# Performance work log

Measured on AMD Instinct MI355X. Metric: run time of the kernel, lower is better.

## Reference

```python
import jax, jax.numpy as jnp
import numpy as np

N, E, G = 50000, 640000, 512
F_NODE, F_EDGE, HID, H, L = 8, 3, 128, 4, 4
C = HID // H


def setup_inputs() -> dict:
    key = jax.random.key(0)
    ks = jax.random.split(key, 24)
    p = lambda k, s: jax.random.normal(k, s, jnp.float32) * 0.1
    return {
        "x": jax.random.normal(ks[0], (N, F_NODE), jnp.float32),
        "edge_attr": jax.random.normal(ks[1], (E, F_EDGE), jnp.float32),
        "edge_index": jax.random.randint(ks[2], (2, E), 0, N, dtype=jnp.int32),
        "batch": jnp.sort(jax.random.randint(ks[3], (N,), 0, G, dtype=jnp.int32)),
        "enc_node_w": p(ks[4], (F_NODE, HID)), "enc_node_b": p(ks[5], (HID,)),
        "enc_edge_w": p(ks[6], (F_EDGE, HID)), "enc_edge_b": p(ks[7], (HID,)),
        "gat_lin_w": p(ks[8], (L, HID, HID)),
        "gat_att_src": p(ks[9], (L, H, C)),
        "gat_att_dst": p(ks[10], (L, H, C)),
        "gat_lin_edge_w": p(ks[11], (L, HID, HID)),
        "gat_att_edge": p(ks[12], (L, H, C)),
        "gat_bias": p(ks[13], (L, HID)),
        "bn_gamma": jnp.ones((L, HID), jnp.float32),
        "bn_beta": jnp.zeros((L, HID), jnp.float32),
        "fc1_w": p(ks[14], (HID, HID)), "fc1_b": p(ks[15], (HID,)),
        "fc2_w": p(ks[16], (HID, HID // 2)), "fc2_b": p(ks[17], (HID // 2,)),
        "fc3_w": p(ks[18], (HID // 2, 1)), "fc3_b": p(ks[19], (1,)),
    }


def _gat(x, src, dst, ea, lin_w, a_src, a_dst, lin_e_w, a_edge, bias):
    # PyG GATConv (concat=True, negative_slope=0.2, edge_dim=HID)
    xp = (x @ lin_w).reshape(N, H, C)                      # [N,H,C]
    s = jnp.einsum('nhc,hc->nh', xp, a_src)                # alpha_src per node
    d = jnp.einsum('nhc,hc->nh', xp, a_dst)                # alpha_dst per node
    ep = (ea @ lin_e_w).reshape(-1, H, C)                  # [Et,H,C]
    e = jnp.einsum('ehc,hc->eh', ep, a_edge)               # alpha_edge per edge
    alpha = jax.nn.leaky_relu(s[src] + d[dst] + e, 0.2)    # [Et,H]
    # segment softmax over incoming edges of each target node
    m = jax.ops.segment_max(alpha, dst, num_segments=N)
    w = jnp.exp(alpha - m[dst])
    z = jax.ops.segment_sum(w, dst, num_segments=N)
    w = w / (z[dst] + 1e-16)
    msg = xp[src] * w[:, :, None]                          # [Et,H,C]
    out = jax.ops.segment_sum(msg, dst, num_segments=N)
    return out.reshape(N, HID) + bias


def reference(x, edge_attr, edge_index, batch,
              enc_node_w, enc_node_b, enc_edge_w, enc_edge_b,
              gat_lin_w, gat_att_src, gat_att_dst, gat_lin_edge_w, gat_att_edge, gat_bias,
              bn_gamma, bn_beta, fc1_w, fc1_b, fc2_w, fc2_b, fc3_w, fc3_b):
    src, dst = edge_index[0], edge_index[1]
    h = x @ enc_node_w + enc_node_b
    ea = edge_attr @ enc_edge_w + enc_edge_b
    # add_self_loops with fill_value='mean': self-loop attr = mean of incoming edge attrs
    deg = jax.ops.segment_sum(jnp.ones((E,), h.dtype), dst, num_segments=N)
    loop_ea = jax.ops.segment_sum(ea, dst, num_segments=N) / jnp.maximum(deg, 1.0)[:, None]
    loop = jnp.arange(N, dtype=src.dtype)
    src_f = jnp.concatenate([src, loop])
    dst_f = jnp.concatenate([dst, loop])
    ea_f = jnp.concatenate([ea, loop_ea], axis=0)
    for i in range(L):
        hn = _gat(h, src_f, dst_f, ea_f, gat_lin_w[i], gat_att_src[i], gat_att_dst[i],
                  gat_lin_edge_w[i], gat_att_edge[i], gat_bias[i])
        mu = hn.mean(0)
        var = ((hn - mu) ** 2).mean(0)                     # BatchNorm1d training-mode stats
        hn = (hn - mu) / jnp.sqrt(var + 1e-5) * bn_gamma[i] + bn_beta[i]
        hn = jax.nn.relu(hn)
        h = h + hn if i > 0 else hn
    # global mean pool over graphs
    cnt = jax.ops.segment_sum(jnp.ones((N,), h.dtype), batch, num_segments=G)
    g = jax.ops.segment_sum(h, batch, num_segments=G) / jnp.maximum(cnt, 1.0)[:, None]
    g = jax.nn.relu(g @ fc1_w + fc1_b)
    g = jax.nn.relu(g @ fc2_w + fc2_b)
    return g @ fc3_w + fc3_b
```

## Files before the change

kernel.cpp:

```cpp
#include <hip/hip_runtime.h>
#include <hip/hip_bf16.h>

#define NN 50000
#define EE 640000
#define ET (EE + NN)
#define GG 512
#define NPB 16
#define NLB 3125
#define CPX 391
#define ECAP 768
#define WSTR (ECAP + 4)

typedef unsigned int uint;
typedef __attribute__((ext_vector_type(8))) short short8;
typedef __attribute__((ext_vector_type(4))) float floatx4;

__device__ inline float2 bf2f(uint u) {
    return make_float2(__uint_as_float(u << 16), __uint_as_float(u & 0xffff0000u));
}
__device__ inline uint packbf(float a, float b) {
    __hip_bfloat162 t;
    t.x = __float2bfloat16(a);
    t.y = __float2bfloat16(b);
    return *(uint*)&t;
}

__global__ __launch_bounds__(256) void k_prep(const float* __restrict__ lin_e_w,
                                              const float* __restrict__ att_e,
                                              const float* __restrict__ encW,
                                              const float* __restrict__ encB,
                                              const float* __restrict__ W,
                                              float* __restrict__ Mt, float* __restrict__ bns4,
                                              uint* __restrict__ WbT) {
    int tid = threadIdx.x;
    if (blockIdx.x == 0) {
        __shared__ float we[128 * 16];
        for (int idx = tid; idx < 2048; idx += 256) {
            int k = idx >> 4, lh = idx & 15, l = lh >> 2, h = lh & 3;
            const float* wrow = lin_e_w + l * 16384 + k * 128 + h * 32;
            const float* arow = att_e + l * 128 + h * 32;
            float acc = 0.f;
#pragma unroll
            for (int c = 0; c < 32; c++) acc += wrow[c] * arow[c];
            we[k * 16 + lh] = acc;
        }
        for (int i = tid; i < 4 * 8 * 256; i += 256) bns4[i] = 0.f;
        __syncthreads();
        if (tid < 64) {
            int lh = tid >> 2, r = tid & 3;
            float acc = 0.f;
            for (int k = 0; k < 128; k++) {
                float a = (r < 3) ? encW[r * 128 + k] : encB[k];
                acc += a * we[k * 16 + lh];
            }
            Mt[lh * 4 + r] = acc;
        }
    } else {
        int idx = (blockIdx.x - 1) * 256 + tid;
        if (idx >= 4 * 128 * 64) return;
        int l = idx >> 13, rem = idx & 8191, n = rem >> 6, u = rem & 63;
        const float* Wl = W + l * 16384;
        WbT[idx] = packbf(Wl[(2 * u) * 128 + n], Wl[(2 * u + 1) * 128 + n]);
    }
}

__global__ __launch_bounds__(256) void k_enc(const float* __restrict__ x,
                                             const float* __restrict__ W,
                                             const float* __restrict__ b,
                                             uint* __restrict__ hb) {
    int idx = blockIdx.x * 256 + threadIdx.x;
    if (idx >= NN * 64) return;
    int n = idx >> 6, c0 = (idx & 63) * 2;
    float a0 = b[c0], a1 = b[c0 + 1];
    const float* xr = x + n * 8;
#pragma unroll
    for (int f = 0; f < 8; f++) {
        a0 += xr[f] * W[f * 128 + c0];
        a1 += xr[f] * W[f * 128 + c0 + 1];
    }
    hb[idx] = packbf(a0, a1);
}

__global__ __launch_bounds__(256) void k_deg(const int* __restrict__ dst, int* __restrict__ deg) {
    int e0 = (blockIdx.x * 256 + threadIdx.x) * 4;
    if (e0 >= EE) return;
    int4 d4 = *(const int4*)(dst + e0);
    atomicAdd(&deg[d4.x], 1);
    atomicAdd(&deg[d4.y], 1);
    atomicAdd(&deg[d4.z], 1);
    atomicAdd(&deg[d4.w], 1);
}

__global__ __launch_bounds__(1024) void k_scan(const int* __restrict__ deg, int* __restrict__ rp,
                                               int* __restrict__ fill) {
    __shared__ int wsum[16];
    __shared__ int carry_sh;
    int tid = threadIdx.x, lane = tid & 63, wid = tid >> 6;
    if (tid == 0) { carry_sh = 0; rp[0] = 0; }
    __syncthreads();
    for (int base = 0; base < NN; base += 8192) {
        int i0 = base + tid * 8;
        int v[8], p[8];
        if (i0 < NN) {
            int4 a = *(const int4*)(deg + i0);
            int4 bq = *(const int4*)(deg + i0 + 4);
            v[0] = a.x + 1; v[1] = a.y + 1; v[2] = a.z + 1; v[3] = a.w + 1;
            v[4] = bq.x + 1; v[5] = bq.y + 1; v[6] = bq.z + 1; v[7] = bq.w + 1;
        } else {
#pragma unroll
            for (int u = 0; u < 8; u++) v[u] = 0;
        }
        int run = 0;
#pragma unroll
        for (int u = 0; u < 8; u++) { run += v[u]; p[u] = run; }
        int xv = run;
        for (int off = 1; off < 64; off <<= 1) {
            int s = __shfl_up(xv, off);
            if (lane >= off) xv += s;
        }
        if (lane == 63) wsum[wid] = xv;
        __syncthreads();
        if (wid == 0 && lane < 16) {
            int s = wsum[lane];
            for (int off = 1; off < 16; off <<= 1) {
                int u = __shfl_up(s, off);
                if (lane >= off) s += u;
            }
            wsum[lane] = s;
        }
        __syncthreads();
        int excl = carry_sh + (wid > 0 ? wsum[wid - 1] : 0) + xv - run;
        if (i0 < NN) {
#pragma unroll
            for (int u = 0; u < 8; u++) {
                rp[i0 + u + 1] = excl + p[u];
                fill[i0 + u] = excl + (u ? p[u - 1] : 0);
            }
        }
        __syncthreads();
        if (tid == 0) carry_sh += wsum[15];
        __syncthreads();
    }
}

__global__ __launch_bounds__(256) void k_fill(const int* __restrict__ src, const int* __restrict__ dst,
                                              const float* __restrict__ edge_attr,
                                              int* __restrict__ fill, int* __restrict__ ed) {
    int e0 = (blockIdx.x * 256 + threadIdx.x) * 4;
    if (e0 >= EE) return;
    int4 d4 = *(const int4*)(dst + e0);
    int4 s4 = *(const int4*)(src + e0);
    const float* ar = edge_attr + (size_t)e0 * 3;
    float4 f0 = *(const float4*)(ar + 0);
    float4 f1 = *(const float4*)(ar + 4);
    float4 f2 = *(const float4*)(ar + 8);
    int p0 = atomicAdd(&fill[d4.x], 1);
    int p1 = atomicAdd(&fill[d4.y], 1);
    int p2 = atomicAdd(&fill[d4.z], 1);
    int p3 = atomicAdd(&fill[d4.w], 1);
    *(int4*)(ed + (size_t)p0 * 4) = make_int4(s4.x, __float_as_int(f0.x), __float_as_int(f0.y), __float_as_int(f0.z));
    *(int4*)(ed + (size_t)p1 * 4) = make_int4(s4.y, __float_as_int(f0.w), __float_as_int(f1.x), __float_as_int(f1.y));
    *(int4*)(ed + (size_t)p2 * 4) = make_int4(s4.z, __float_as_int(f1.z), __float_as_int(f1.w), __float_as_int(f2.x));
    *(int4*)(ed + (size_t)p3 * 4) = make_int4(s4.w, __float_as_int(f2.y), __float_as_int(f2.z), __float_as_int(f2.w));
}

__global__ __launch_bounds__(256) void k_selfloop(const int* __restrict__ rp, int* __restrict__ ed) {
    int t = blockIdx.x * 256 + threadIdx.x;
    int n = t >> 4, sub = t & 15;
    if (n >= NN) return;
    int b = rp[n], en = rp[n + 1];
    int d = en - b - 1;
    float s0 = 0.f, s1 = 0.f, s2 = 0.f;
    for (int j = sub; j < d; j += 16) {
        int4 r = *(const int4*)(ed + (size_t)(b + j) * 4);
        s0 += __int_as_float(r.y); s1 += __int_as_float(r.z); s2 += __int_as_float(r.w);
    }
#pragma unroll
    for (int off = 8; off; off >>= 1) {
        s0 += __shfl_xor(s0, off, 16);
        s1 += __shfl_xor(s1, off, 16);
        s2 += __shfl_xor(s2, off, 16);
    }
    if (sub == 0) {
        float inv = 1.f / fmaxf((float)d, 1.f);
        *(int4*)(ed + (size_t)(en - 1) * 4) =
            make_int4(n, __float_as_int(s0 * inv), __float_as_int(s1 * inv), __float_as_int(s2 * inv));
    }
}

__global__ __launch_bounds__(256) void k_gemm(const uint* __restrict__ hb, const uint* __restrict__ WbT,
                                              const float* __restrict__ a_src, const float* __restrict__ a_dst,
                                              uint* __restrict__ xpb, float* __restrict__ s_arr,
                                              float* __restrict__ d_arr) {
    __shared__ __align__(16) uint Bl[128 * 68];
    int tid = threadIdx.x;
    for (int idx = tid; idx < 2048; idx += 256) {
        int n = idx >> 4, u4 = idx & 15;
        uint4 v = *(const uint4*)(WbT + n * 64 + u4 * 4);
        *(uint4*)(&Bl[n * 68 + u4 * 4]) = v;
    }
    int lane = tid & 63, wv = tid >> 6;
    int ln15 = lane & 15, quad = lane >> 4;
    int rowBase = blockIdx.x * 64 + wv * 16;
    int rowA = rowBase + ln15;
    int rowAc = rowA < NN ? rowA : 0;
    __syncthreads();
    short8 af[4];
#pragma unroll
    for (int c = 0; c < 4; c++)
        af[c] = *(const short8*)((const short*)hb + (size_t)rowAc * 128 + c * 32 + quad * 8);
    floatx4 acc[8];
#pragma unroll
    for (int t = 0; t < 8; t++) acc[t] = (floatx4){0.f, 0.f, 0.f, 0.f};
#pragma unroll
    for (int c = 0; c < 4; c++) {
#pragma unroll
        for (int t = 0; t < 8; t++) {
            short8 bf = *(const short8*)((const short*)&Bl[(16 * t + ln15) * 68] + c * 32 + quad * 8);
            acc[t] = __builtin_amdgcn_mfma_f32_16x16x32_bf16(af[c], bf, acc[t], 0, 0, 0);
        }
    }
#pragma unroll
    for (int t = 0; t < 8; t++) {
#pragma unroll
        for (int r = 0; r < 4; r++) {
            float v = acc[t][r];
            float vhi = __shfl_xor(v, 1);
            int grow = rowBase + quad * 4 + r;
            if (!(ln15 & 1) && grow < NN)
                xpb[(size_t)grow * 64 + 8 * t + (ln15 >> 1)] = packbf(v, vhi);
        }
    }
    float asl[4], ash[4], adl[4], adh[4];
#pragma unroll
    for (int hh = 0; hh < 4; hh++) {
        asl[hh] = a_src[hh * 32 + ln15]; ash[hh] = a_src[hh * 32 + 16 + ln15];
        adl[hh] = a_dst[hh * 32 + ln15]; adh[hh] = a_dst[hh * 32 + 16 + ln15];
    }
#pragma unroll
    for (int r = 0; r < 4; r++) {
        float s0 = acc[0][r] * asl[0] + acc[1][r] * ash[0];
        float s1 = acc[2][r] * asl[1] + acc[3][r] * ash[1];
        float s2 = acc[4][r] * asl[2] + acc[5][r] * ash[2];
        float s3 = acc[6][r] * asl[3] + acc[7][r] * ash[3];
        float d0 = acc[0][r] * adl[0] + acc[1][r] * adh[0];
        float d1 = acc[2][r] * adl[1] + acc[3][r] * adh[1];
        float d2 = acc[4][r] * adl[2] + acc[5][r] * adh[2];
        float d3 = acc[6][r] * adl[3] + acc[7][r] * adh[3];
#pragma unroll
        for (int off = 1; off < 16; off <<= 1) {
            s0 += __shfl_xor(s0, off); s1 += __shfl_xor(s1, off);
            s2 += __shfl_xor(s2, off); s3 += __shfl_xor(s3, off);
            d0 += __shfl_xor(d0, off); d1 += __shfl_xor(d1, off);
            d2 += __shfl_xor(d2, off); d3 += __shfl_xor(d3, off);
        }
        int grow = rowBase + quad * 4 + r;
        if (ln15 == 0 && grow < NN) {
            *(float4*)(s_arr + grow * 4) = make_float4(s0, s1, s2, s3);
            *(float4*)(d_arr + grow * 4) = make_float4(d0, d1, d2, d3);
        }
    }
}

__global__ __launch_bounds__(256) void k_edge(const int* __restrict__ rp, const int* __restrict__ ed,
                                              const float* __restrict__ Mt,
                                              const float* __restrict__ s_arr, const float* __restrict__ d_arr,
                                              const uint* __restrict__ xpb, uint* __restrict__ outb,
                                              float* __restrict__ bns, int layer) {
    __shared__ int rps[NPB + 1];
    __shared__ float d4c[NPB][4];
    __shared__ __align__(16) float shw[4][WSTR];
    __shared__ int shs[ECAP];
    int tid = threadIdx.x;
    int lb = (blockIdx.x & 7) * CPX + (blockIdx.x >> 3);
    if (lb >= NLB) return;
    int nb0 = lb * NPB;
    if (tid <= NPB) rps[tid] = rp[nb0 + tid];
    if (tid < NPB * 4)
        d4c[tid >> 2][tid & 3] = d_arr[(size_t)(nb0 + (tid >> 2)) * 4 + (tid & 3)];
    float4 mt0 = *(const float4*)(Mt + (layer * 4 + 0) * 4);
    float4 mt1 = *(const float4*)(Mt + (layer * 4 + 1) * 4);
    float4 mt2 = *(const float4*)(Mt + (layer * 4 + 2) * 4);
    float4 mt3 = *(const float4*)(Mt + (layer * 4 + 3) * 4);
    __syncthreads();
    int e0 = rps[0], e1 = rps[NPB];
    int e1c = e1 - e0 > ECAP ? e0 + ECAP : e1;
    for (int s = e0 + tid; s < e1c; s += 256) {
        int lo = 0, hi = NPB - 1;
        while (lo < hi) { int mid = (lo + hi) >> 1; if (rps[mid + 1] <= s) lo = mid + 1; else hi = mid; }
        int ni = lo;
        int4 r = *(const int4*)(ed + (size_t)s * 4);
        int sv = r.x;
        float a0 = __int_as_float(r.y), a1 = __int_as_float(r.z), a2 = __int_as_float(r.w);
        int kni = rps[ni + 1] - rps[ni];
        float wf = (s == rps[ni + 1] - 1) ? (kni > 1 ? 1.f : 0.f) : 1.f;
        float4 s4 = *(const float4*)(s_arr + (size_t)sv * 4);
        float e_0 = a0 * mt0.x + a1 * mt0.y + a2 * mt0.z + wf * mt0.w;
        float e_1 = a0 * mt1.x + a1 * mt1.y + a2 * mt1.z + wf * mt1.w;
        float e_2 = a0 * mt2.x + a1 * mt2.y + a2 * mt2.z + wf * mt2.w;
        float e_3 = a0 * mt3.x + a1 * mt3.y + a2 * mt3.z + wf * mt3.w;
        float al0 = s4.x + d4c[ni][0] + e_0; al0 = al0 > 0.f ? al0 : 0.2f * al0;
        float al1 = s4.y + d4c[ni][1] + e_1; al1 = al1 > 0.f ? al1 : 0.2f * al1;
        float al2 = s4.z + d4c[ni][2] + e_2; al2 = al2 > 0.f ? al2 : 0.2f * al2;
        float al3 = s4.w + d4c[ni][3] + e_3; al3 = al3 > 0.f ? al3 : 0.2f * al3;
        int ls = s - e0;
        shs[ls] = sv;
        shw[0][ls] = __expf(al0);
        shw[1][ls] = __expf(al1);
        shw[2][ls] = __expf(al2);
        shw[3][ls] = __expf(al3);
    }
    __syncthreads();
    int wv = tid >> 6, lane = tid & 63, hh = lane >> 4;
    float4 mth = hh == 0 ? mt0 : hh == 1 ? mt1 : hh == 2 ? mt2 : mt3;
    float bs0 = 0.f, bs1 = 0.f, bq0 = 0.f, bq1 = 0.f;
#pragma unroll
    for (int q = 0; q < 4; q++) {
        int ni = wv * 4 + q;
        int startg = rps[ni];
        int start = startg - e0;
        int k = rps[ni + 1] - startg;
        float acc0 = 0.f, acc1 = 0.f, z = 0.f;
        int kc = ECAP - start;
        kc = kc < 0 ? 0 : (kc > k ? k : kc);
        int j = 0;
        for (; j + 4 <= kc; j += 4) {
            int s0 = shs[start + j], s1 = shs[start + j + 1];
            int s2 = shs[start + j + 2], s3 = shs[start + j + 3];
            float w0 = shw[hh][start + j], w1 = shw[hh][start + j + 1];
            float w2 = shw[hh][start + j + 2], w3 = shw[hh][start + j + 3];
            z += w0 + w1 + w2 + w3;
            uint x0 = xpb[(size_t)s0 * 64 + lane];
            uint x1 = xpb[(size_t)s1 * 64 + lane];
            uint x2 = xpb[(size_t)s2 * 64 + lane];
            uint x3 = xpb[(size_t)s3 * 64 + lane];
            float2 f0 = bf2f(x0), f1 = bf2f(x1), f2 = bf2f(x2), f3 = bf2f(x3);
            acc0 += w0 * f0.x + w1 * f1.x + w2 * f2.x + w3 * f3.x;
            acc1 += w0 * f0.y + w1 * f1.y + w2 * f2.y + w3 * f3.y;
        }
        for (; j < kc; j++) {
            float w = shw[hh][start + j];
            int sv = shs[start + j];
            z += w;
            float2 f = bf2f(xpb[(size_t)sv * 64 + lane]);
            acc0 += w * f.x; acc1 += w * f.y;
        }
        for (; j < k; j++) {
            int sg = startg + j;
            int4 r = *(const int4*)(ed + (size_t)sg * 4);
            int sv = r.x;
            float a0 = __int_as_float(r.y), a1 = __int_as_float(r.z), a2 = __int_as_float(r.w);
            float wf = (j < k - 1) ? 1.f : (k > 1 ? 1.f : 0.f);
            float sva = s_arr[(size_t)sv * 4 + hh];
            float ev = a0 * mth.x + a1 * mth.y + a2 * mth.z + wf * mth.w;
            float a = sva + d4c[ni][hh] + ev; a = a > 0.f ? a : 0.2f * a;
            float w = __expf(a);
            z += w;
            float2 f = bf2f(xpb[(size_t)sv * 64 + lane]);
            acc0 += w * f.x; acc1 += w * f.y;
        }
        float zi = 1.f / (z + 1e-16f);
        float o0 = acc0 * zi, o1 = acc1 * zi;
        outb[(size_t)(nb0 + ni) * 64 + lane] = packbf(o0, o1);
        bs0 += o0; bs1 += o1; bq0 += o0 * o0; bq1 += o1 * o1;
    }
    __syncthreads();
    float* scratch = &shw[0][0];
    scratch[wv * 256 + lane * 4 + 0] = bs0;
    scratch[wv * 256 + lane * 4 + 1] = bs1;
    scratch[wv * 256 + lane * 4 + 2] = bq0;
    scratch[wv * 256 + lane * 4 + 3] = bq1;
    __syncthreads();
    float v = scratch[tid] + scratch[256 + tid] + scratch[512 + tid] + scratch[768 + tid];
    int ln = tid >> 2, st = tid & 3;
    int gidx = (st < 2) ? (2 * ln + st) : (128 + 2 * ln + (st - 2));
    atomicAdd(&bns[(blockIdx.x & 7) * 256 + gidx], v);
}

__global__ __launch_bounds__(256) void k_norm(const uint* __restrict__ xb, const float* __restrict__ sums,
                                              const float* __restrict__ gamma, const float* __restrict__ beta,
                                              uint* __restrict__ hb, int first) {
    __shared__ float sc[128], sf[128];
    int tid = threadIdx.x;
    if (tid < 128) {
        float s = 0.f, q = 0.f;
#pragma unroll
        for (int k = 0; k < 8; k++) { s += sums[k * 256 + tid]; q += sums[k * 256 + 128 + tid]; }
        float mu = s * (1.f / NN);
        float var = q * (1.f / NN) - mu * mu;
        float iv = rsqrtf(fmaxf(var, 0.f) + 1e-5f);
        float a = gamma[tid] * iv;
        sc[tid] = a;
        sf[tid] = beta[tid] - mu * a;
    }
    __syncthreads();
    int idx = blockIdx.x * 256 + tid;
    if (idx >= NN * 64) return;
    int c0 = (idx & 63) * 2;
    float2 v2 = bf2f(xb[idx]);
    float r0 = fmaxf(v2.x * sc[c0] + sf[c0], 0.f);
    float r1 = fmaxf(v2.y * sc[c0 + 1] + sf[c0 + 1], 0.f);
    if (!first) {
        float2 hp = bf2f(hb[idx]);
        r0 += hp.x; r1 += hp.y;
    }
    hb[idx] = packbf(r0, r1);
}

__global__ __launch_bounds__(256) void k_pool(const uint* __restrict__ hb, const int* __restrict__ batch,
                                              float* __restrict__ g) {
    int t = threadIdx.x & 63, rh = threadIdx.x >> 6;
    int gi = blockIdx.x;
    int lo = 0, hi = NN;
    while (lo < hi) { int mid = (lo + hi) >> 1; if (batch[mid] < gi) lo = mid + 1; else hi = mid; }
    int start = lo;
    hi = NN;
    while (lo < hi) { int mid = (lo + hi) >> 1; if (batch[mid] < gi + 1) lo = mid + 1; else hi = mid; }
    int end = lo;
    float s0 = 0.f, s1 = 0.f;
    for (int n = start + rh; n < end; n += 4) {
        float2 v = bf2f(hb[(size_t)n * 64 + t]);
        s0 += v.x; s1 += v.y;
    }
    __shared__ float sh[2][256];
    sh[0][threadIdx.x] = s0; sh[1][threadIdx.x] = s1;
    __syncthreads();
    if (rh == 0) {
        float inv = 1.f / fmaxf((float)(end - start), 1.f);
        g[gi * 128 + 2 * t]     = (sh[0][t] + sh[0][64 + t] + sh[0][128 + t] + sh[0][192 + t]) * inv;
        g[gi * 128 + 2 * t + 1] = (sh[1][t] + sh[1][64 + t] + sh[1][128 + t] + sh[1][192 + t]) * inv;
    }
}

__global__ __launch_bounds__(128) void k_fc(const float* __restrict__ g,
                                            const float* __restrict__ w1, const float* __restrict__ b1,
                                            const float* __restrict__ w2, const float* __restrict__ b2,
                                            const float* __restrict__ w3, const float* __restrict__ b3,
                                            float* __restrict__ out) {
    __shared__ float gv[128];
    __shared__ float h1[128];
    __shared__ float h2[64];
    int gi = blockIdx.x, t = threadIdx.x;
    gv[t] = g[gi * 128 + t];
    __syncthreads();
    float acc = b1[t];
    for (int kk = 0; kk < 128; kk++) acc += gv[kk] * w1[kk * 128 + t];
    h1[t] = fmaxf(acc, 0.f);
    __syncthreads();
    if (t < 64) {
        float a2 = b2[t];
        for (int kk = 0; kk < 128; kk++) a2 += h1[kk] * w2[kk * 64 + t];
        h2[t] = fmaxf(a2, 0.f);
    }
    __syncthreads();
    if (t < 64) {
        float p = h2[t] * w3[t];
#pragma unroll
        for (int off = 32; off; off >>= 1) p += __shfl_xor(p, off);
        if (t == 0) out[gi] = p + b3[0];
    }
}

extern "C" void kernel_launch(void* const* d_in, const int* in_sizes, int n_in,
                              void* d_out, int out_size, void* d_ws, size_t ws_size,
                              hipStream_t stream) {
    const float* x            = (const float*)d_in[0];
    const float* edge_attr    = (const float*)d_in[1];
    const int*   edge_index   = (const int*)d_in[2];
    const int*   batch        = (const int*)d_in[3];
    const float* enc_node_w   = (const float*)d_in[4];
    const float* enc_node_b   = (const float*)d_in[5];
    const float* enc_edge_w   = (const float*)d_in[6];
    const float* enc_edge_b   = (const float*)d_in[7];
    const float* gat_lin_w    = (const float*)d_in[8];
    const float* gat_att_src  = (const float*)d_in[9];
    const float* gat_att_dst  = (const float*)d_in[10];
    const float* gat_lin_edge = (const float*)d_in[11];
    const float* gat_att_edge = (const float*)d_in[12];
    const float* bn_gamma     = (const float*)d_in[14];
    const float* bn_beta      = (const float*)d_in[15];
    const float* fc1_w        = (const float*)d_in[16];
    const float* fc1_b        = (const float*)d_in[17];
    const float* fc2_w        = (const float*)d_in[18];
    const float* fc2_b        = (const float*)d_in[19];
    const float* fc3_w        = (const float*)d_in[20];
    const float* fc3_b        = (const float*)d_in[21];
    float* outv = (float*)d_out;

    char* ws = (char*)d_ws;
    size_t off = 0;
    auto alloc = [&](size_t bytes) -> void* {
        void* p = ws + off;
        off = (off + bytes + 255) & ~(size_t)255;
        return p;
    };
    uint*  hbv     = (uint*)alloc((size_t)NN * 64 * 4);
    uint*  goutb   = (uint*)alloc((size_t)NN * 64 * 4);
    uint*  xpb     = (uint*)alloc((size_t)NN * 64 * 4);
    float* s_arr   = (float*)alloc((size_t)NN * 4 * 4);
    float* d_arr   = (float*)alloc((size_t)NN * 4 * 4);
    int*   deg     = (int*)alloc((size_t)NN * 4);
    int*   fill    = (int*)alloc((size_t)NN * 4);
    int*   rp      = (int*)alloc((size_t)(NN + 1) * 4);
    int*   ed      = (int*)alloc((size_t)ET * 4 * 4);
    uint*  WbT     = (uint*)alloc((size_t)4 * 128 * 64 * 4);
    float* Mt      = (float*)alloc(64 * 4);
    float* bns4    = (float*)alloc((size_t)4 * 8 * 256 * 4);
    float* g       = (float*)alloc((size_t)GG * 128 * 4);
    (void)ws_size; (void)in_sizes; (void)n_in; (void)out_size;

    hipMemsetAsync(deg, 0, NN * 4, stream);

    const int* srce = edge_index;
    const int* dste = edge_index + EE;

    k_prep<<<1 + (4 * 128 * 64 + 255) / 256, 256, 0, stream>>>(gat_lin_edge, gat_att_edge,
                                                               enc_edge_w, enc_edge_b, gat_lin_w,
                                                               Mt, bns4, WbT);
    k_enc<<<(NN * 64 + 255) / 256, 256, 0, stream>>>(x, enc_node_w, enc_node_b, hbv);
    k_deg<<<(EE / 4 + 255) / 256, 256, 0, stream>>>(dste, deg);
    k_scan<<<1, 1024, 0, stream>>>(deg, rp, fill);
    k_fill<<<(EE / 4 + 255) / 256, 256, 0, stream>>>(srce, dste, edge_attr, fill, ed);
    k_selfloop<<<(NN * 16 + 255) / 256, 256, 0, stream>>>(rp, ed);

    for (int l = 0; l < 4; l++) {
        k_gemm<<<(NN + 63) / 64, 256, 0, stream>>>(hbv, WbT + l * 8192,
                                                   gat_att_src + l * 128, gat_att_dst + l * 128,
                                                   xpb, s_arr, d_arr);
        k_edge<<<8 * CPX, 256, 0, stream>>>(rp, ed, Mt, s_arr, d_arr, xpb, goutb,
                                            bns4 + l * 2048, l);
        k_norm<<<(NN * 64 + 255) / 256, 256, 0, stream>>>(goutb, bns4 + l * 2048, bn_gamma + l * 128,
                                                          bn_beta + l * 128, hbv, l == 0 ? 1 : 0);
    }

    k_pool<<<GG, 256, 0, stream>>>(hbv, batch, g);
    k_fc<<<GG, 128, 0, stream>>>(g, fc1_w, fc1_b, fc2_w, fc2_b, fc3_w, fc3_b, outv);
}
```

Baseline: 484.6 us.

## Fuse BatchNorm/residual into next GEMM and pooling/FC tail, merge encoder into prep

Removes the per-layer k_norm pass by applying BatchNorm, ReLU and the residual add inside the next layer's GEMM prologue, which also writes the updated hidden state and stages it in shared memory. The last layer's normalisation is fused into a combined pooling+MLP kernel, and the node encoder is folded into the prep kernel. The degree and fill kernels now process 8 edges per thread. Together this cuts kernel launches and one full read/write pass over node features per layer. In exchange the GEMM needs more shared memory and the tail recomputes the normalisation while reading two arrays.

```diff
diff --git a/kernel.cpp b/kernel.cpp
--- a/kernel.cpp
+++ b/kernel.cpp
@@ -30,10 +30,14 @@
                                               const float* __restrict__ encW,
                                               const float* __restrict__ encB,
                                               const float* __restrict__ W,
+                                              const float* __restrict__ x,
+                                              const float* __restrict__ nodeW,
+                                              const float* __restrict__ nodeB,
                                               float* __restrict__ Mt, float* __restrict__ bns4,
-                                              uint* __restrict__ WbT) {
+                                              uint* __restrict__ WbT, uint* __restrict__ hb) {
     int tid = threadIdx.x;
-    if (blockIdx.x == 0) {
+    int blk = blockIdx.x;
+    if (blk == 0) {
         __shared__ float we[128 * 16];
         for (int idx = tid; idx < 2048; idx += 256) {
             int k = idx >> 4, lh = idx & 15, l = lh >> 2, h = lh & 3;
@@ -55,40 +59,34 @@
             }
             Mt[lh * 4 + r] = acc;
         }
-    } else {
-        int idx = (blockIdx.x - 1) * 256 + tid;
-        if (idx >= 4 * 128 * 64) return;
+    } else if (blk <= 128) {
+        int idx = (blk - 1) * 256 + tid;
         int l = idx >> 13, rem = idx & 8191, n = rem >> 6, u = rem & 63;
         const float* Wl = W + l * 16384;
         WbT[idx] = packbf(Wl[(2 * u) * 128 + n], Wl[(2 * u + 1) * 128 + n]);
-    }
-}
-
-__global__ __launch_bounds__(256) void k_enc(const float* __restrict__ x,
-                                             const float* __restrict__ W,
-                                             const float* __restrict__ b,
-                                             uint* __restrict__ hb) {
-    int idx = blockIdx.x * 256 + threadIdx.x;
-    if (idx >= NN * 64) return;
-    int n = idx >> 6, c0 = (idx & 63) * 2;
-    float a0 = b[c0], a1 = b[c0 + 1];
-    const float* xr = x + n * 8;
-#pragma unroll
-    for (int f = 0; f < 8; f++) {
-        a0 += xr[f] * W[f * 128 + c0];
-        a1 += xr[f] * W[f * 128 + c0 + 1];
-    }
-    hb[idx] = packbf(a0, a1);
+    } else {
+        int idx = (blk - 129) * 256 + tid;
+        if (idx >= NN * 64) return;
+        int n = idx >> 6, c0 = (idx & 63) * 2;
+        float a0 = nodeB[c0], a1 = nodeB[c0 + 1];
+        const float* xr = x + n * 8;
+#pragma unroll
+        for (int f = 0; f < 8; f++) {
+            a0 += xr[f] * nodeW[f * 128 + c0];
+            a1 += xr[f] * nodeW[f * 128 + c0 + 1];
+        }
+        hb[idx] = packbf(a0, a1);
+    }
 }
 
 __global__ __launch_bounds__(256) void k_deg(const int* __restrict__ dst, int* __restrict__ deg) {
-    int e0 = (blockIdx.x * 256 + threadIdx.x) * 4;
+    int e0 = (blockIdx.x * 256 + threadIdx.x) * 8;
     if (e0 >= EE) return;
-    int4 d4 = *(const int4*)(dst + e0);
-    atomicAdd(&deg[d4.x], 1);
-    atomicAdd(&deg[d4.y], 1);
-    atomicAdd(&deg[d4.z], 1);
-    atomicAdd(&deg[d4.w], 1);
+    int4 d0 = *(const int4*)(dst + e0), d1 = *(const int4*)(dst + e0 + 4);
+    atomicAdd(&deg[d0.x], 1); atomicAdd(&deg[d0.y], 1);
+    atomicAdd(&deg[d0.z], 1); atomicAdd(&deg[d0.w], 1);
+    atomicAdd(&deg[d1.x], 1); atomicAdd(&deg[d1.y], 1);
+    atomicAdd(&deg[d1.z], 1); atomicAdd(&deg[d1.w], 1);
 }
 
 __global__ __launch_bounds__(1024) void k_scan(const int* __restrict__ deg, int* __restrict__ rp,
@@ -146,22 +144,25 @@
 __global__ __launch_bounds__(256) void k_fill(const int* __restrict__ src, const int* __restrict__ dst,
                                               const float* __restrict__ edge_attr,
                                               int* __restrict__ fill, int* __restrict__ ed) {
-    int e0 = (blockIdx.x * 256 + threadIdx.x) * 4;
+    int e0 = (blockIdx.x * 256 + threadIdx.x) * 8;
     if (e0 >= EE) return;
-    int4 d4 = *(const int4*)(dst + e0);
-    int4 s4 = *(const int4*)(src + e0);
-    const float* ar = edge_attr + (size_t)e0 * 3;
-    float4 f0 = *(const float4*)(ar + 0);
-    float4 f1 = *(const float4*)(ar + 4);
-    float4 f2 = *(const float4*)(ar + 8);
-    int p0 = atomicAdd(&fill[d4.x], 1);
-    int p1 = atomicAdd(&fill[d4.y], 1);
-    int p2 = atomicAdd(&fill[d4.z], 1);
-    int p3 = atomicAdd(&fill[d4.w], 1);
-    *(int4*)(ed + (size_t)p0 * 4) = make_int4(s4.x, __float_as_int(f0.x), __float_as_int(f0.y), __float_as_int(f0.z));
-    *(int4*)(ed + (size_t)p1 * 4) = make_int4(s4.y, __float_as_int(f0.w), __float_as_int(f1.x), __float_as_int(f1.y));
-    *(int4*)(ed + (size_t)p2 * 4) = make_int4(s4.z, __float_as_int(f1.z), __float_as_int(f1.w), __float_as_int(f2.x));
-    *(int4*)(ed + (size_t)p3 * 4) = make_int4(s4.w, __float_as_int(f2.y), __float_as_int(f2.z), __float_as_int(f2.w));
+    int4 d0 = *(const int4*)(dst + e0), d1 = *(const int4*)(dst + e0 + 4);
+    int4 s0 = *(const int4*)(src + e0), s1 = *(const int4*)(src + e0 + 4);
+    const float4* ar4 = (const float4*)(edge_attr + (size_t)e0 * 3);
+    float4 q[6];
+#pragma unroll
+    for (int i = 0; i < 6; i++) q[i] = ar4[i];
+    const float* a = (const float*)q;
+    int dd[8] = {d0.x, d0.y, d0.z, d0.w, d1.x, d1.y, d1.z, d1.w};
+    int ss[8] = {s0.x, s0.y, s0.z, s0.w, s1.x, s1.y, s1.z, s1.w};
+    int pp[8];
+#pragma unroll
+    for (int i = 0; i < 8; i++) pp[i] = atomicAdd(&fill[dd[i]], 1);
+#pragma unroll
+    for (int i = 0; i < 8; i++)
+        *(int4*)(ed + (size_t)pp[i] * 4) =
+            make_int4(ss[i], __float_as_int(a[3 * i]), __float_as_int(a[3 * i + 1]),
+                      __float_as_int(a[3 * i + 2]));
 }
 
 __global__ __launch_bounds__(256) void k_selfloop(const int* __restrict__ rp, int* __restrict__ ed) {
@@ -188,27 +189,72 @@
     }
 }
 
-__global__ __launch_bounds__(256) void k_gemm(const uint* __restrict__ hb, const uint* __restrict__ WbT,
+__global__ __launch_bounds__(256) void k_gemm(uint* __restrict__ hb, const uint* __restrict__ gout,
+                                              const float* __restrict__ bns,
+                                              const float* __restrict__ gamma,
+                                              const float* __restrict__ beta,
+                                              const uint* __restrict__ WbT,
                                               const float* __restrict__ a_src, const float* __restrict__ a_dst,
                                               uint* __restrict__ xpb, float* __restrict__ s_arr,
-                                              float* __restrict__ d_arr) {
+                                              float* __restrict__ d_arr, int mode) {
     __shared__ __align__(16) uint Bl[128 * 68];
+    __shared__ __align__(16) uint Ah[64 * 66];
+    __shared__ float sc[128], sf[128];
     int tid = threadIdx.x;
+    int rowBase = blockIdx.x * 64;
     for (int idx = tid; idx < 2048; idx += 256) {
         int n = idx >> 4, u4 = idx & 15;
         uint4 v = *(const uint4*)(WbT + n * 64 + u4 * 4);
         *(uint4*)(&Bl[n * 68 + u4 * 4]) = v;
     }
+    if (mode && tid < 128) {
+        float s = 0.f, q = 0.f;
+#pragma unroll
+        for (int k = 0; k < 8; k++) { s += bns[k * 256 + tid]; q += bns[k * 256 + 128 + tid]; }
+        float mu = s * (1.f / NN);
+        float var = q * (1.f / NN) - mu * mu;
+        float iv = rsqrtf(fmaxf(var, 0.f) + 1e-5f);
+        float a = gamma[tid] * iv;
+        sc[tid] = a;
+        sf[tid] = beta[tid] - mu * a;
+    }
+    __syncthreads();
+    if (mode) {
+        for (int idx = tid; idx < 4096; idx += 256) {
+            int row = idx >> 6, u = idx & 63;
+            int gr = rowBase + row;
+            uint pk = 0;
+            if (gr < NN) {
+                float2 v = bf2f(gout[(size_t)gr * 64 + u]);
+                int c0 = u * 2;
+                float r0 = fmaxf(v.x * sc[c0] + sf[c0], 0.f);
+                float r1 = fmaxf(v.y * sc[c0 + 1] + sf[c0 + 1], 0.f);
+                if (mode == 2) {
+                    float2 hp = bf2f(hb[(size_t)gr * 64 + u]);
+                    r0 += hp.x; r1 += hp.y;
+                }
+                pk = packbf(r0, r1);
+                hb[(size_t)gr * 64 + u] = pk;
+            }
+            Ah[row * 66 + u] = pk;
+        }
+        __syncthreads();
+    }
     int lane = tid & 63, wv = tid >> 6;
     int ln15 = lane & 15, quad = lane >> 4;
-    int rowBase = blockIdx.x * 64 + wv * 16;
-    int rowA = rowBase + ln15;
-    int rowAc = rowA < NN ? rowA : 0;
-    __syncthreads();
+    int rowL = wv * 16 + ln15;
+    int rowA = rowBase + rowL;
     short8 af[4];
-#pragma unroll
-    for (int c = 0; c < 4; c++)
-        af[c] = *(const short8*)((const short*)hb + (size_t)rowAc * 128 + c * 32 + quad * 8);
+    if (mode) {
+#pragma unroll
+        for (int c = 0; c < 4; c++)
+            af[c] = *(const short8*)((const short*)&Ah[rowL * 66] + c * 32 + quad * 8);
+    } else {
+        int rowAc = rowA < NN ? rowA : 0;
+#pragma unroll
+        for (int c = 0; c < 4; c++)
+            af[c] = *(const short8*)((const short*)hb + (size_t)rowAc * 128 + c * 32 + quad * 8);
+    }
     floatx4 acc[8];
 #pragma unroll
     for (int t = 0; t < 8; t++) acc[t] = (floatx4){0.f, 0.f, 0.f, 0.f};
@@ -226,7 +272,7 @@
         for (int r = 0; r < 4; r++) {
             float v = acc[t][r];
             float vhi = __shfl_xor(v, 1);
-            int grow = rowBase + quad * 4 + r;
+            int grow = rowBase + wv * 16 + quad * 4 + r;
             if (!(ln15 & 1) && grow < NN)
                 xpb[(size_t)grow * 64 + 8 * t + (ln15 >> 1)] = packbf(v, vhi);
         }
@@ -254,7 +300,7 @@
             d0 += __shfl_xor(d0, off); d1 += __shfl_xor(d1, off);
             d2 += __shfl_xor(d2, off); d3 += __shfl_xor(d3, off);
         }
-        int grow = rowBase + quad * 4 + r;
+        int grow = rowBase + wv * 16 + quad * 4 + r;
         if (ln15 == 0 && grow < NN) {
             *(float4*)(s_arr + grow * 4) = make_float4(s0, s1, s2, s3);
             *(float4*)(d_arr + grow * 4) = make_float4(d0, d1, d2, d3);
@@ -377,15 +423,22 @@
     atomicAdd(&bns[(blockIdx.x & 7) * 256 + gidx], v);
 }
 
-__global__ __launch_bounds__(256) void k_norm(const uint* __restrict__ xb, const float* __restrict__ sums,
+__global__ __launch_bounds__(256) void k_tail(const uint* __restrict__ hb, const uint* __restrict__ gout,
+                                              const float* __restrict__ bns,
                                               const float* __restrict__ gamma, const float* __restrict__ beta,
-                                              uint* __restrict__ hb, int first) {
+                                              const int* __restrict__ batch,
+                                              const float* __restrict__ w1, const float* __restrict__ b1,
+                                              const float* __restrict__ w2, const float* __restrict__ b2,
+                                              const float* __restrict__ w3, const float* __restrict__ b3,
+                                              float* __restrict__ out) {
     __shared__ float sc[128], sf[128];
+    __shared__ float sh[2][256];
+    __shared__ float gv[128], h1[128], h2[64];
     int tid = threadIdx.x;
     if (tid < 128) {
         float s = 0.f, q = 0.f;
 #pragma unroll
-        for (int k = 0; k < 8; k++) { s += sums[k * 256 + tid]; q += sums[k * 256 + 128 + tid]; }
+        for (int k = 0; k < 8; k++) { s += bns[k * 256 + tid]; q += bns[k * 256 + 128 + tid]; }
         float mu = s * (1.f / NN);
         float var = q * (1.f / NN) - mu * mu;
         float iv = rsqrtf(fmaxf(var, 0.f) + 1e-5f);
@@ -394,23 +447,8 @@
         sf[tid] = beta[tid] - mu * a;
     }
     __syncthreads();
-    int idx = blockIdx.x * 256 + tid;
-    if (idx >= NN * 64) return;
-    int c0 = (idx & 63) * 2;
-    float2 v2 = bf2f(xb[idx]);
-    float r0 = fmaxf(v2.x * sc[c0] + sf[c0], 0.f);
-    float r1 = fmaxf(v2.y * sc[c0 + 1] + sf[c0 + 1], 0.f);
-    if (!first) {
-        float2 hp = bf2f(hb[idx]);
-        r0 += hp.x; r1 += hp.y;
-    }
-    hb[idx] = packbf(r0, r1);
-}
-
-__global__ __launch_bounds__(256) void k_pool(const uint* __restrict__ hb, const int* __restrict__ batch,
-                                              float* __restrict__ g) {
-    int t = threadIdx.x & 63, rh = threadIdx.x >> 6;
     int gi = blockIdx.x;
+    int t = tid & 63, rh = tid >> 6;
     int lo = 0, hi = NN;
     while (lo < hi) { int mid = (lo + hi) >> 1; if (batch[mid] < gi) lo = mid + 1; else hi = mid; }
     int start = lo;
@@ -418,46 +456,39 @@
     while (lo < hi) { int mid = (lo + hi) >> 1; if (batch[mid] < gi + 1) lo = mid + 1; else hi = mid; }
     int end = lo;
     float s0 = 0.f, s1 = 0.f;
+    int c0 = t * 2;
+    float a0c = sc[c0], a1c = sc[c0 + 1], f0c = sf[c0], f1c = sf[c0 + 1];
     for (int n = start + rh; n < end; n += 4) {
-        float2 v = bf2f(hb[(size_t)n * 64 + t]);
-        s0 += v.x; s1 += v.y;
-    }
-    __shared__ float sh[2][256];
-    sh[0][threadIdx.x] = s0; sh[1][threadIdx.x] = s1;
+        float2 gvv = bf2f(gout[(size_t)n * 64 + t]);
+        float2 hp = bf2f(hb[(size_t)n * 64 + t]);
+        s0 += hp.x + fmaxf(gvv.x * a0c + f0c, 0.f);
+        s1 += hp.y + fmaxf(gvv.y * a1c + f1c, 0.f);
+    }
+    sh[0][tid] = s0; sh[1][tid] = s1;
     __syncthreads();
     if (rh == 0) {
         float inv = 1.f / fmaxf((float)(end - start), 1.f);
-        g[gi * 128 + 2 * t]     = (sh[0][t] + sh[0][64 + t] + sh[0][128 + t] + sh[0][192 + t]) * inv;
-        g[gi * 128 + 2 * t + 1] = (sh[1][t] + sh[1][64 + t] + sh[1][128 + t] + sh[1][192 + t]) * inv;
-    }
-}
-
-__global__ __launch_bounds__(128) void k_fc(const float* __restrict__ g,
-                                            const float* __restrict__ w1, const float* __restrict__ b1,
-                                            const float* __restrict__ w2, const float* __restrict__ b2,
-                                            const float* __restrict__ w3, const float* __restrict__ b3,
-                                            float* __restrict__ out) {
-    __shared__ float gv[128];
-    __shared__ float h1[128];
-    __shared__ float h2[64];
-    int gi = blockIdx.x, t = threadIdx.x;
-    gv[t] = g[gi * 128 + t];
-    __syncthreads();
-    float acc = b1[t];
-    for (int kk = 0; kk < 128; kk++) acc += gv[kk] * w1[kk * 128 + t];
-    h1[t] = fmaxf(acc, 0.f);
-    __syncthreads();
-    if (t < 64) {
-        float a2 = b2[t];
-        for (int kk = 0; kk < 128; kk++) a2 += h1[kk] * w2[kk * 64 + t];
-        h2[t] = fmaxf(a2, 0.f);
-    }
-    __syncthreads();
-    if (t < 64) {
-        float p = h2[t] * w3[t];
+        gv[2 * t]     = (sh[0][t] + sh[0][64 + t] + sh[0][128 + t] + sh[0][192 + t]) * inv;
+        gv[2 * t + 1] = (sh[1][t] + sh[1][64 + t] + sh[1][128 + t] + sh[1][192 + t]) * inv;
+    }
+    __syncthreads();
+    if (tid < 128) {
+        float acc = b1[tid];
+        for (int kk = 0; kk < 128; kk++) acc += gv[kk] * w1[kk * 128 + tid];
+        h1[tid] = fmaxf(acc, 0.f);
+    }
+    __syncthreads();
+    if (tid < 64) {
+        float a2 = b2[tid];
+        for (int kk = 0; kk < 128; kk++) a2 += h1[kk] * w2[kk * 64 + tid];
+        h2[tid] = fmaxf(a2, 0.f);
+    }
+    __syncthreads();
+    if (tid < 64) {
+        float p = h2[tid] * w3[tid];
 #pragma unroll
         for (int off = 32; off; off >>= 1) p += __shfl_xor(p, off);
-        if (t == 0) out[gi] = p + b3[0];
+        if (tid == 0) out[gi] = p + b3[0];
     }
 }
 
@@ -506,7 +537,6 @@
     uint*  WbT     = (uint*)alloc((size_t)4 * 128 * 64 * 4);
     float* Mt      = (float*)alloc(64 * 4);
     float* bns4    = (float*)alloc((size_t)4 * 8 * 256 * 4);
-    float* g       = (float*)alloc((size_t)GG * 128 * 4);
     (void)ws_size; (void)in_sizes; (void)n_in; (void)out_size;
 
     hipMemsetAsync(deg, 0, NN * 4, stream);
@@ -514,25 +544,30 @@
     const int* srce = edge_index;
     const int* dste = edge_index + EE;
 
-    k_prep<<<1 + (4 * 128 * 64 + 255) / 256, 256, 0, stream>>>(gat_lin_edge, gat_att_edge,
-                                                               enc_edge_w, enc_edge_b, gat_lin_w,
-                                                               Mt, bns4, WbT);
-    k_enc<<<(NN * 64 + 255) / 256, 256, 0, stream>>>(x, enc_node_w, enc_node_b, hbv);
-    k_deg<<<(EE / 4 + 255) / 256, 256, 0, stream>>>(dste, deg);
+    k_prep<<<129 + (NN * 64 + 255) / 256, 256, 0, stream>>>(gat_lin_edge, gat_att_edge,
+                                                            enc_edge_w, enc_edge_b, gat_lin_w,
+                                                            x, enc_node_w, enc_node_b,
+                                                            Mt, bns4, WbT, hbv);
+    k_deg<<<(EE / 8 + 255) / 256, 256, 0, stream>>>(dste, deg);
     k_scan<<<1, 1024, 0, stream>>>(deg, rp, fill);
-    k_fill<<<(EE / 4 + 255) / 256, 256, 0, stream>>>(srce, dste, edge_attr, fill, ed);
+    k_fill<<<(EE / 8 + 255) / 256, 256, 0, stream>>>(srce, dste, edge_attr, fill, ed);
     k_selfloop<<<(NN * 16 + 255) / 256, 256, 0, stream>>>(rp, ed);
 
     for (int l = 0; l < 4; l++) {
-        k_gemm<<<(NN + 63) / 64, 256, 0, stream>>>(hbv, WbT + l * 8192,
+        int mode = (l == 0) ? 0 : (l == 1 ? 1 : 2);
+        const float* bnsPrev = bns4 + (l - 1) * 2048;
+        k_gemm<<<(NN + 63) / 64, 256, 0, stream>>>(hbv, goutb,
+                                                   mode ? bnsPrev : bns4,
+                                                   bn_gamma + (l ? (l - 1) * 128 : 0),
+                                                   bn_beta + (l ? (l - 1) * 128 : 0),
+                                                   WbT + l * 8192,
                                                    gat_att_src + l * 128, gat_att_dst + l * 128,
-                                                   xpb, s_arr, d_arr);
+                                                   xpb, s_arr, d_arr, mode);
         k_edge<<<8 * CPX, 256, 0, stream>>>(rp, ed, Mt, s_arr, d_arr, xpb, goutb,
                                             bns4 + l * 2048, l);
-        k_norm<<<(NN * 64 + 255) / 256, 256, 0, stream>>>(goutb, bns4 + l * 2048, bn_gamma + l * 128,
-                                                          bn_beta + l * 128, hbv, l == 0 ? 1 : 0);
-    }
-
-    k_pool<<<GG, 256, 0, stream>>>(hbv, batch, g);
-    k_fc<<<GG, 128, 0, stream>>>(g, fc1_w, fc1_b, fc2_w, fc2_b, fc3_w, fc3_b, outv);
-}
+    }
+
+    k_tail<<<GG, 256, 0, stream>>>(hbv, goutb, bns4 + 3 * 2048, bn_gamma + 3 * 128,
+                                   bn_beta + 3 * 128, batch,
+                                   fc1_w, fc1_b, fc2_w, fc2_b, fc3_w, fc3_b, outv);
+}
```

Result: no change. 482.0 us (-0.5%).
